# Performance work log

Hardware: AMD Instinct MI355X
Metric: run time of the kernel (lower is better)

Reference implementation:

```python
import jax, jax.numpy as jnp
import numpy as np

IGNORE_INDEX = -100
B, S, D, V = 4, 2048, 2048, 32000


def setup_inputs() -> dict:
    key = jax.random.key(0)
    k1, k2, k3, k4 = jax.random.split(key, 4)
    hidden = jax.random.normal(k1, (B, S, D), dtype=jnp.float32)
    targets = jax.random.randint(k2, (B, S), 0, V, dtype=jnp.int64)
    drop = jax.random.uniform(k3, (B, S)) < 0.1
    targets = jnp.where(drop, IGNORE_INDEX, targets)
    W = jax.random.normal(k4, (V, D), dtype=jnp.float32) * (D ** -0.5)
    return {"hidden": hidden, "targets": targets, "W": W}


def reference(hidden, targets, W):
    # hidden: [B, S, D], targets: [B, S] int, W: [V, D]
    mask = targets != IGNORE_INDEX                      # [B, S]
    total = mask.sum()
    # Linear projection to vocab, CE computed in fp32 (matches logits.float())
    logits = jnp.einsum('bsd,vd->bsv', hidden, W).astype(jnp.float32)  # [B, S, V]
    logp = jax.nn.log_softmax(logits, axis=-1)
    safe_t = jnp.where(mask, targets, 0)
    nll = -jnp.take_along_axis(logp, safe_t[..., None], axis=-1)[..., 0]  # [B, S]
    loss_sum = jnp.sum(jnp.where(mask, nll, 0.0))
    return loss_sum / total.astype(jnp.float32)
```

## Files before the change

### kernel.cpp

```cpp
#include <hip/hip_runtime.h>
#include <hip/hip_bf16.h>
#include <stdint.h>

#define IGNORE_INDEX (-100)

constexpr int M_ = 8192;
constexpr int K_ = 2048;
constexpr int N_ = 32000;

constexpr int BM = 128, BN = 128;

typedef __attribute__((ext_vector_type(4)))  float f32x4;
typedef __attribute__((ext_vector_type(16))) float f32x16;
typedef __attribute__((ext_vector_type(4)))  int   i32x4;
typedef __attribute__((ext_vector_type(8)))  int   i32x8;
typedef __attribute__((ext_vector_type(4)))  unsigned int u32x4;
typedef __attribute__((ext_vector_type(8)))  __bf16 bf16x8;

#define SCALE_A 8.0f
#define SCALE_W 1024.0f
#define INV_S   (1.0f / (8.0f * 1024.0f))

__device__ __forceinline__ unsigned pack_bf16(float f0, float f1) {
    unsigned u0 = __builtin_bit_cast(unsigned, f0) + 0x8000u;
    unsigned u1 = __builtin_bit_cast(unsigned, f1) + 0x8000u;
    return __builtin_amdgcn_perm(u1, u0, 0x07060302u);
}
__device__ __forceinline__ u32x4 pack8(f32x4 lo, f32x4 hi) {
    u32x4 r;
    r[0] = pack_bf16(lo[0], lo[1]);
    r[1] = pack_bf16(lo[2], lo[3]);
    r[2] = pack_bf16(hi[0], hi[1]);
    r[3] = pack_bf16(hi[2], hi[3]);
    return r;
}

__device__ __forceinline__ void gll16(const void* g, void* l) {
    __builtin_amdgcn_global_load_lds(
        (const __attribute__((address_space(1))) unsigned int*)g,
        (__attribute__((address_space(3))) unsigned int*)l, 16, 0, 0);
}

__global__ void init_acc(float* p, int n) {
    int i = blockIdx.x * 256 + threadIdx.x;
    if (i < n) p[i] = 0.0f;
}

__global__ __launch_bounds__(256) void convert_fp8(
    const float* __restrict__ in, unsigned int* __restrict__ out,
    float scale, int n8)
{
    int i = blockIdx.x * 256 + threadIdx.x;
    if (i < n8) {
        f32x4 lo = ((const f32x4*)in)[2 * i];
        f32x4 hi = ((const f32x4*)in)[2 * i + 1];
        int w0 = 0, w1 = 0;
        w0 = __builtin_amdgcn_cvt_pk_fp8_f32(lo[0] * scale, lo[1] * scale, w0, false);
        w0 = __builtin_amdgcn_cvt_pk_fp8_f32(lo[2] * scale, lo[3] * scale, w0, true);
        w1 = __builtin_amdgcn_cvt_pk_fp8_f32(hi[0] * scale, hi[1] * scale, w1, false);
        w1 = __builtin_amdgcn_cvt_pk_fp8_f32(hi[2] * scale, hi[3] * scale, w1, true);
        out[2 * i]     = (unsigned int)w0;
        out[2 * i + 1] = (unsigned int)w1;
    }
}

__global__ __launch_bounds__(512, 3) void gemm_fp8(
    const unsigned char* __restrict__ A,
    const unsigned char* __restrict__ Wq,
    const int*   __restrict__ tgt,
    float* __restrict__ sumexp,
    float* __restrict__ tgtlogit)
{
    __shared__ __align__(16) unsigned char As[BM * 64];
    __shared__ __align__(16) unsigned char Bs[BN * 64];
    __shared__ int tg[BM];

    const int tid = threadIdx.x;
    const int mt  = blockIdx.x;
    const int nt  = blockIdx.y;

    if (tid < BM) tg[tid] = tgt[mt * BM + tid];

    const int wave = tid >> 6;
    const int lane = tid & 63;
    const int wmo  = (wave & 3) * 32;
    const int wno  = (wave >> 2) * 64;

    const int srow = tid >> 2;
    const int spg  = (tid & 3) ^ ((srow >> 1) & 3);
    const unsigned char* gA = A  + (size_t)(mt * BM + srow) * K_ + spg * 16;
    const unsigned char* gB = Wq + (size_t)(nt * BN + srow) * K_ + spg * 16;
    unsigned char* lA = &As[wave * 1024];
    unsigned char* lB = &Bs[wave * 1024];

    const int l31 = lane & 31;
    const int h   = lane >> 5;
    const int ra  = wmo + l31;
    const int rb0 = wno + l31;
    const int rb1 = wno + 32 + l31;
    const int xa  = (ra  >> 1) & 3;
    const int xb0 = (rb0 >> 1) & 3;
    const int xb1 = (rb1 >> 1) & 3;
    const unsigned char* fA0 = &As[ra  * 64 + ((2 * h)     ^ xa ) * 16];
    const unsigned char* fA1 = &As[ra  * 64 + ((2 * h + 1) ^ xa ) * 16];
    const unsigned char* fB00 = &Bs[rb0 * 64 + ((2 * h)     ^ xb0) * 16];
    const unsigned char* fB01 = &Bs[rb0 * 64 + ((2 * h + 1) ^ xb0) * 16];
    const unsigned char* fB10 = &Bs[rb1 * 64 + ((2 * h)     ^ xb1) * 16];
    const unsigned char* fB11 = &Bs[rb1 * 64 + ((2 * h + 1) ^ xb1) * 16];

    f32x16 acc0, acc1;
#pragma unroll
    for (int r = 0; r < 16; r++) { acc0[r] = 0.f; acc1[r] = 0.f; }

#pragma unroll 1
    for (int kt = 0; kt < K_; kt += 64) {
        gll16(gA + kt, lA);
        gll16(gB + kt, lB);
        __syncthreads();

        i32x4 a_lo = *(const i32x4*)fA0;
        i32x4 a_hi = *(const i32x4*)fA1;
        i32x4 b0lo = *(const i32x4*)fB00;
        i32x4 b0hi = *(const i32x4*)fB01;
        i32x4 b1lo = *(const i32x4*)fB10;
        i32x4 b1hi = *(const i32x4*)fB11;
        i32x8 af = (i32x8){a_lo[0], a_lo[1], a_lo[2], a_lo[3],
                           a_hi[0], a_hi[1], a_hi[2], a_hi[3]};
        i32x8 bf0 = (i32x8){b0lo[0], b0lo[1], b0lo[2], b0lo[3],
                            b0hi[0], b0hi[1], b0hi[2], b0hi[3]};
        i32x8 bf1 = (i32x8){b1lo[0], b1lo[1], b1lo[2], b1lo[3],
                            b1hi[0], b1hi[1], b1hi[2], b1hi[3]};

        acc0 = __builtin_amdgcn_mfma_scale_f32_32x32x64_f8f6f4(
            af, bf0, acc0, 0, 0, 0, 0x7F7F7F7F, 0, 0x7F7F7F7F);
        acc1 = __builtin_amdgcn_mfma_scale_f32_32x32x64_f8f6f4(
            af, bf1, acc1, 0, 0, 0, 0x7F7F7F7F, 0, 0x7F7F7F7F);

        __syncthreads();
    }

    const int c0 = nt * BN + wno + l31;
#pragma unroll
    for (int reg = 0; reg < 16; reg++) {
        const int lrow = wmo + (reg & 3) + 8 * (reg >> 2) + 4 * h;
        const int grow = mt * BM + lrow;
        const int t    = tg[lrow];
        float v0 = acc0[reg] * INV_S;
        float v1 = acc1[reg] * INV_S;
        if (t == c0)      tgtlogit[grow] = v0;
        if (t == c0 + 32) tgtlogit[grow] = v1;
        float rs = __expf(v0) + __expf(v1);
        rs += __shfl_xor(rs, 1);
        rs += __shfl_xor(rs, 2);
        rs += __shfl_xor(rs, 4);
        rs += __shfl_xor(rs, 8);
        rs += __shfl_xor(rs, 16);
        if (l31 == 0) atomicAdd(&sumexp[grow], rs);
    }
}

constexpr int BKf = 32;
constexpr int LDA = BKf + 8;
__global__ __launch_bounds__(256) void gemm_fused_f32(
    const float* __restrict__ A,
    const float* __restrict__ W,
    const int*   __restrict__ tgt,
    float* __restrict__ sumexp,
    float* __restrict__ tgtlogit)
{
    __shared__ __bf16 As[BM * LDA];
    __shared__ __bf16 Bs[BN * LDA];
    __shared__ int    tg[BM];

    const int tid = threadIdx.x;
    const int mt  = blockIdx.x;
    const int nt  = blockIdx.y;
    if (tid < BM) tg[tid] = tgt[mt * BM + tid];

    const int wave = tid >> 6, lane = tid & 63;
    const int wm = wave >> 1, wn = wave & 1;
    const int lquad = lane >> 4, lcol = lane & 15;
    const int srow = tid >> 2, scol = (tid & 3) * 8;

    const float* gA = A + (size_t)(mt * BM + srow) * K_ + scol;
    const float* gB = W + (size_t)(nt * BN + srow) * K_ + scol;
    const size_t rowstep = (size_t)64 * K_;

    f32x4 acc[4][4];
#pragma unroll
    for (int i = 0; i < 4; i++)
#pragma unroll
        for (int j = 0; j < 4; j++) acc[i][j] = (f32x4){0.f, 0.f, 0.f, 0.f};

    for (int kt = 0; kt < K_; kt += BKf) {
        f32x4 a0 = *(const f32x4*)(gA + kt);
        f32x4 a1 = *(const f32x4*)(gA + kt + 4);
        f32x4 a2 = *(const f32x4*)(gA + kt + rowstep);
        f32x4 a3 = *(const f32x4*)(gA + kt + rowstep + 4);
        f32x4 b0 = *(const f32x4*)(gB + kt);
        f32x4 b1 = *(const f32x4*)(gB + kt + 4);
        f32x4 b2 = *(const f32x4*)(gB + kt + rowstep);
        f32x4 b3 = *(const f32x4*)(gB + kt + rowstep + 4);
        __syncthreads();
        *(u32x4*)&As[srow * LDA + scol]        = pack8(a0, a1);
        *(u32x4*)&As[(srow + 64) * LDA + scol] = pack8(a2, a3);
        *(u32x4*)&Bs[srow * LDA + scol]        = pack8(b0, b1);
        *(u32x4*)&Bs[(srow + 64) * LDA + scol] = pack8(b2, b3);
        __syncthreads();
        bf16x8 af[4], bf[4];
#pragma unroll
        for (int f = 0; f < 4; f++) {
            af[f] = *(const bf16x8*)&As[(wm * 64 + f * 16 + lcol) * LDA + lquad * 8];
            bf[f] = *(const bf16x8*)&Bs[(wn * 64 + f * 16 + lcol) * LDA + lquad * 8];
        }
#pragma unroll
        for (int mf = 0; mf < 4; mf++)
#pragma unroll
            for (int nf = 0; nf < 4; nf++)
                acc[mf][nf] = __builtin_amdgcn_mfma_f32_16x16x32_bf16(af[mf], bf[nf], acc[mf][nf], 0, 0, 0);
    }
    const int colbase = nt * BN + wn * 64;
#pragma unroll
    for (int mf = 0; mf < 4; mf++) {
#pragma unroll
        for (int r = 0; r < 4; r++) {
            const int lrow = wm * 64 + mf * 16 + lquad * 4 + r;
            const int grow = mt * BM + lrow;
            const int t    = tg[lrow];
            float rs = 0.f;
#pragma unroll
            for (int nf = 0; nf < 4; nf++) {
                float v = acc[mf][nf][r];
                rs += __expf(v);
                if (t == colbase + nf * 16 + lcol) tgtlogit[grow] = v;
            }
            rs += __shfl_xor(rs, 1);
            rs += __shfl_xor(rs, 2);
            rs += __shfl_xor(rs, 4);
            rs += __shfl_xor(rs, 8);
            if (lcol == 0) atomicAdd(&sumexp[grow], rs);
        }
    }
}

__global__ __launch_bounds__(256) void finalize(
    const float* __restrict__ sumexp,
    const float* __restrict__ tgtlogit,
    const int*   __restrict__ tgt,
    float* __restrict__ out)
{
    float s = 0.f;
    int   c = 0;
    for (int i = threadIdx.x; i < M_; i += 256) {
        int t = tgt[i];
        if (t != IGNORE_INDEX) {
            s += __logf(sumexp[i]) - tgtlogit[i];
            c++;
        }
    }
#pragma unroll
    for (int o = 32; o; o >>= 1) {
        s += __shfl_down(s, o);
        c += __shfl_down(c, o);
    }
    __shared__ float ss[4];
    __shared__ int   cc[4];
    int w = threadIdx.x >> 6;
    if ((threadIdx.x & 63) == 0) { ss[w] = s; cc[w] = c; }
    __syncthreads();
    if (threadIdx.x == 0) {
        float st = ss[0] + ss[1] + ss[2] + ss[3];
        int   ct = cc[0] + cc[1] + cc[2] + cc[3];
        out[0] = st / (float)ct;
    }
}

extern "C" void kernel_launch(void* const* d_in, const int* in_sizes, int n_in,
                              void* d_out, int out_size, void* d_ws, size_t ws_size,
                              hipStream_t stream) {
    const float* hidden  = (const float*)d_in[0];
    const int*   targets = (const int*)d_in[1];
    const float* W       = (const float*)d_in[2];

    float* sumexp   = (float*)d_ws;
    float* tgtlogit = sumexp + M_;
    float* out      = (float*)d_out;

    unsigned char* Aq = (unsigned char*)d_ws + 2 * M_ * sizeof(float);
    unsigned char* Wq = Aq + (size_t)M_ * K_;
    const size_t need = 2 * M_ * sizeof(float) + (size_t)M_ * K_ + (size_t)N_ * K_;

    init_acc<<<(2 * M_ + 255) / 256, 256, 0, stream>>>(sumexp, 2 * M_);

    if (ws_size >= need) {
        const int a8 = M_ * K_ / 8;
        const int w8 = N_ * K_ / 8;
        convert_fp8<<<(a8 + 255) / 256, 256, 0, stream>>>(hidden, (unsigned int*)Aq, SCALE_A, a8);
        convert_fp8<<<(w8 + 255) / 256, 256, 0, stream>>>(W, (unsigned int*)Wq, SCALE_W, w8);
        gemm_fp8<<<dim3(M_ / BM, N_ / BN), 512, 0, stream>>>(Aq, Wq, targets, sumexp, tgtlogit);
    } else {
        gemm_fused_f32<<<dim3(M_ / BM, N_ / BN), 256, 0, stream>>>(hidden, W, targets, sumexp, tgtlogit);
    }

    finalize<<<1, 256, 0, stream>>>(sumexp, tgtlogit, targets, out);
}
```

Baseline: 1.101 ms.

## Double-buffer fp8 GEMM LDS tiles and use 2x2 MFMA tiles per wave

Restructures the fp8 GEMM to use 256 threads with each wave computing a 64x64 sub-tile through four MFMAs, which raises register-level reuse of A and B fragments. LDS is double-buffered so the global-to-LDS loads for the next K slice are issued before computing the current one, aiming to hide memory latency behind MFMA work. It also raises wave priority around the MFMA block. The trade is more accumulator registers and twice the LDS per block, which may reduce occupancy.

```diff
diff --git a/kernel.cpp b/kernel.cpp
--- a/kernel.cpp
+++ b/kernel.cpp
@@ -64,15 +64,56 @@
     }
 }
 
-__global__ __launch_bounds__(512, 3) void gemm_fp8(
+
+#define MFMA_SC(a, b, c) \
+    __builtin_amdgcn_mfma_scale_f32_32x32x64_f8f6f4( \
+        (a), (b), (c), 0, 0, 0, 0x7F7F7F7F, 0, 0x7F7F7F7F)
+
+#define STAGE(asb, bsb, koff)                          \
+    do {                                               \
+        gll16(gA0 + (koff), (asb) + stoff);            \
+        gll16(gA1 + (koff), (asb) + stoff + 4096);     \
+        gll16(gB0 + (koff), (bsb) + stoff);            \
+        gll16(gB1 + (koff), (bsb) + stoff + 4096);     \
+    } while (0)
+
+#define COMPUTE(asb, bsb)                                                     \
+    do {                                                                      \
+        const unsigned char* pA_ = (asb);                                     \
+        const unsigned char* pB_ = (bsb);                                     \
+        i32x4 aL0 = *(const i32x4*)(pA_ + aoffL);                             \
+        i32x4 aH0 = *(const i32x4*)(pA_ + aoffH);                             \
+        i32x4 aL1 = *(const i32x4*)(pA_ + aoffL + 2048);                      \
+        i32x4 aH1 = *(const i32x4*)(pA_ + aoffH + 2048);                      \
+        i32x4 bL0 = *(const i32x4*)(pB_ + boffL);                             \
+        i32x4 bH0 = *(const i32x4*)(pB_ + boffH);                             \
+        i32x4 bL1 = *(const i32x4*)(pB_ + boffL + 2048);                      \
+        i32x4 bH1 = *(const i32x4*)(pB_ + boffH + 2048);                      \
+        i32x8 af0 = (i32x8){aL0[0], aL0[1], aL0[2], aL0[3],                   \
+                            aH0[0], aH0[1], aH0[2], aH0[3]};                  \
+        i32x8 af1 = (i32x8){aL1[0], aL1[1], aL1[2], aL1[3],                   \
+                            aH1[0], aH1[1], aH1[2], aH1[3]};                  \
+        i32x8 bf0 = (i32x8){bL0[0], bL0[1], bL0[2], bL0[3],                   \
+                            bH0[0], bH0[1], bH0[2], bH0[3]};                  \
+        i32x8 bf1 = (i32x8){bL1[0], bL1[1], bL1[2], bL1[3],                   \
+                            bH1[0], bH1[1], bH1[2], bH1[3]};                  \
+        __builtin_amdgcn_s_setprio(1);                                        \
+        acc00 = MFMA_SC(af0, bf0, acc00);                                     \
+        acc01 = MFMA_SC(af0, bf1, acc01);                                     \
+        acc10 = MFMA_SC(af1, bf0, acc10);                                     \
+        acc11 = MFMA_SC(af1, bf1, acc11);                                     \
+        __builtin_amdgcn_s_setprio(0);                                        \
+    } while (0)
+
+__global__ __launch_bounds__(256, 3) void gemm_fp8(
     const unsigned char* __restrict__ A,
     const unsigned char* __restrict__ Wq,
     const int*   __restrict__ tgt,
     float* __restrict__ sumexp,
     float* __restrict__ tgtlogit)
 {
-    __shared__ __align__(16) unsigned char As[BM * 64];
-    __shared__ __align__(16) unsigned char Bs[BN * 64];
+    __shared__ __align__(16) unsigned char As[2][BM * 64];
+    __shared__ __align__(16) unsigned char Bs[2][BN * 64];
     __shared__ int tg[BM];
 
     const int tid = threadIdx.x;
@@ -83,79 +124,86 @@
 
     const int wave = tid >> 6;
     const int lane = tid & 63;
-    const int wmo  = (wave & 3) * 32;
-    const int wno  = (wave >> 2) * 64;
+    const int wm   = wave >> 1;
+    const int wn   = wave & 1;
 
     const int srow = tid >> 2;
     const int spg  = (tid & 3) ^ ((srow >> 1) & 3);
-    const unsigned char* gA = A  + (size_t)(mt * BM + srow) * K_ + spg * 16;
-    const unsigned char* gB = Wq + (size_t)(nt * BN + srow) * K_ + spg * 16;
-    unsigned char* lA = &As[wave * 1024];
-    unsigned char* lB = &Bs[wave * 1024];
+    const unsigned char* gA0 = A  + (size_t)(mt * BM + srow) * K_ + spg * 16;
+    const unsigned char* gB0 = Wq + (size_t)(nt * BN + srow) * K_ + spg * 16;
+    const unsigned char* gA1 = gA0 + (size_t)64 * K_;
+    const unsigned char* gB1 = gB0 + (size_t)64 * K_;
+    const int stoff = wave * 1024;
 
     const int l31 = lane & 31;
     const int h   = lane >> 5;
-    const int ra  = wmo + l31;
-    const int rb0 = wno + l31;
-    const int rb1 = wno + 32 + l31;
-    const int xa  = (ra  >> 1) & 3;
-    const int xb0 = (rb0 >> 1) & 3;
-    const int xb1 = (rb1 >> 1) & 3;
-    const unsigned char* fA0 = &As[ra  * 64 + ((2 * h)     ^ xa ) * 16];
-    const unsigned char* fA1 = &As[ra  * 64 + ((2 * h + 1) ^ xa ) * 16];
-    const unsigned char* fB00 = &Bs[rb0 * 64 + ((2 * h)     ^ xb0) * 16];
-    const unsigned char* fB01 = &Bs[rb0 * 64 + ((2 * h + 1) ^ xb0) * 16];
-    const unsigned char* fB10 = &Bs[rb1 * 64 + ((2 * h)     ^ xb1) * 16];
-    const unsigned char* fB11 = &Bs[rb1 * 64 + ((2 * h + 1) ^ xb1) * 16];
-
-    f32x16 acc0, acc1;
-#pragma unroll
-    for (int r = 0; r < 16; r++) { acc0[r] = 0.f; acc1[r] = 0.f; }
+    const int ra  = wm * 64 + l31;
+    const int rb  = wn * 64 + l31;
+    const int xa  = (ra >> 1) & 3;
+    const int xb  = (rb >> 1) & 3;
+    const int aoffL = ra * 64 + ((2 * h)     ^ xa) * 16;
+    const int aoffH = ra * 64 + ((2 * h + 1) ^ xa) * 16;
+    const int boffL = rb * 64 + ((2 * h)     ^ xb) * 16;
+    const int boffH = rb * 64 + ((2 * h + 1) ^ xb) * 16;
+
+    f32x16 acc00, acc01, acc10, acc11;
+#pragma unroll
+    for (int r = 0; r < 16; r++) {
+        acc00[r] = 0.f; acc01[r] = 0.f; acc10[r] = 0.f; acc11[r] = 0.f;
+    }
+
+    STAGE(As[0], Bs[0], 0);
+    __syncthreads();
 
 #pragma unroll 1
-    for (int kt = 0; kt < K_; kt += 64) {
-        gll16(gA + kt, lA);
-        gll16(gB + kt, lB);
+    for (int kt = 0; kt < K_; kt += 128) {
+        STAGE(As[1], Bs[1], kt + 64);
+        __builtin_amdgcn_sched_barrier(0);
+        COMPUTE(As[0], Bs[0]);
         __syncthreads();
 
-        i32x4 a_lo = *(const i32x4*)fA0;
-        i32x4 a_hi = *(const i32x4*)fA1;
-        i32x4 b0lo = *(const i32x4*)fB00;
-        i32x4 b0hi = *(const i32x4*)fB01;
-        i32x4 b1lo = *(const i32x4*)fB10;
-        i32x4 b1hi = *(const i32x4*)fB11;
-        i32x8 af = (i32x8){a_lo[0], a_lo[1], a_lo[2], a_lo[3],
-                           a_hi[0], a_hi[1], a_hi[2], a_hi[3]};
-        i32x8 bf0 = (i32x8){b0lo[0], b0lo[1], b0lo[2], b0lo[3],
-                            b0hi[0], b0hi[1], b0hi[2], b0hi[3]};
-        i32x8 bf1 = (i32x8){b1lo[0], b1lo[1], b1lo[2], b1lo[3],
-                            b1hi[0], b1hi[1], b1hi[2], b1hi[3]};
-
-        acc0 = __builtin_amdgcn_mfma_scale_f32_32x32x64_f8f6f4(
-            af, bf0, acc0, 0, 0, 0, 0x7F7F7F7F, 0, 0x7F7F7F7F);
-        acc1 = __builtin_amdgcn_mfma_scale_f32_32x32x64_f8f6f4(
-            af, bf1, acc1, 0, 0, 0, 0x7F7F7F7F, 0, 0x7F7F7F7F);
-
+        if (kt + 128 < K_) STAGE(As[0], Bs[0], kt + 128);
+        __builtin_amdgcn_sched_barrier(0);
+        COMPUTE(As[1], Bs[1]);
         __syncthreads();
     }
 
-    const int c0 = nt * BN + wno + l31;
+    const int c0 = nt * BN + wn * 64 + l31;
 #pragma unroll
     for (int reg = 0; reg < 16; reg++) {
-        const int lrow = wmo + (reg & 3) + 8 * (reg >> 2) + 4 * h;
-        const int grow = mt * BM + lrow;
-        const int t    = tg[lrow];
-        float v0 = acc0[reg] * INV_S;
-        float v1 = acc1[reg] * INV_S;
-        if (t == c0)      tgtlogit[grow] = v0;
-        if (t == c0 + 32) tgtlogit[grow] = v1;
-        float rs = __expf(v0) + __expf(v1);
-        rs += __shfl_xor(rs, 1);
-        rs += __shfl_xor(rs, 2);
-        rs += __shfl_xor(rs, 4);
-        rs += __shfl_xor(rs, 8);
-        rs += __shfl_xor(rs, 16);
-        if (l31 == 0) atomicAdd(&sumexp[grow], rs);
+        const int rbase = (reg & 3) + 8 * (reg >> 2) + 4 * h;
+        {
+            const int lrow = wm * 64 + rbase;
+            const int grow = mt * BM + lrow;
+            const int t    = tg[lrow];
+            float v0 = acc00[reg] * INV_S;
+            float v1 = acc01[reg] * INV_S;
+            if (t == c0)      tgtlogit[grow] = v0;
+            if (t == c0 + 32) tgtlogit[grow] = v1;
+            float rs = __expf(v0) + __expf(v1);
+            rs += __shfl_xor(rs, 1);
+            rs += __shfl_xor(rs, 2);
+            rs += __shfl_xor(rs, 4);
+            rs += __shfl_xor(rs, 8);
+            rs += __shfl_xor(rs, 16);
+            if (l31 == 0) atomicAdd(&sumexp[grow], rs);
+        }
+        {
+            const int lrow = wm * 64 + 32 + rbase;
+            const int grow = mt * BM + lrow;
+            const int t    = tg[lrow];
+            float v0 = acc10[reg] * INV_S;
+            float v1 = acc11[reg] * INV_S;
+            if (t == c0)      tgtlogit[grow] = v0;
+            if (t == c0 + 32) tgtlogit[grow] = v1;
+            float rs = __expf(v0) + __expf(v1);
+            rs += __shfl_xor(rs, 1);
+            rs += __shfl_xor(rs, 2);
+            rs += __shfl_xor(rs, 4);
+            rs += __shfl_xor(rs, 8);
+            rs += __shfl_xor(rs, 16);
+            if (l31 == 0) atomicAdd(&sumexp[grow], rs);
+        }
     }
 }
 
@@ -297,7 +345,7 @@
         const int w8 = N_ * K_ / 8;
         convert_fp8<<<(a8 + 255) / 256, 256, 0, stream>>>(hidden, (unsigned int*)Aq, SCALE_A, a8);
         convert_fp8<<<(w8 + 255) / 256, 256, 0, stream>>>(W, (unsigned int*)Wq, SCALE_W, w8);
-        gemm_fp8<<<dim3(M_ / BM, N_ / BN), 512, 0, stream>>>(Aq, Wq, targets, sumexp, tgtlogit);
+        gemm_fp8<<<dim3(M_ / BM, N_ / BN), 256, 0, stream>>>(Aq, Wq, targets, sumexp, tgtlogit);
     } else {
         gemm_fused_f32<<<dim3(M_ / BM, N_ / BN), 256, 0, stream>>>(hidden, W, targets, sumexp, tgtlogit);
     }
```

New measurement: 1.082 ms. No clear change (-1.7%).

## Enlarge FP8 GEMM tile to 256x256 with double-buffered pipelined LDS loads

Applied to the files above, without the earlier changes.

Reworks the FP8 MFMA GEMM to use 256x256 block tiles, with each wave computing a 128x64 sub-tile (4x2 MFMAs). LDS is double-buffered so global-to-LDS loads for the next k-tile are issued between MFMA groups, using fine-grained barriers, waitcnts and setprio. The 1D grid is remapped so consecutive blocks are spread across XCDs. This targets the old kernel's low arithmetic intensity and its full sync stalls on every k-step. In exchange it uses more registers and LDS (occupancy drops to 2 blocks), and the hand-written barrier and waitcnt ordering is fragile.

```diff
diff --git a/kernel.cpp b/kernel.cpp
--- a/kernel.cpp
+++ b/kernel.cpp
@@ -7,8 +7,6 @@
 constexpr int M_ = 8192;
 constexpr int K_ = 2048;
 constexpr int N_ = 32000;
-
-constexpr int BM = 128, BN = 128;
 
 typedef __attribute__((ext_vector_type(4)))  float f32x4;
 typedef __attribute__((ext_vector_type(16))) float f32x16;
@@ -64,101 +62,187 @@
     }
 }
 
-__global__ __launch_bounds__(512, 3) void gemm_fp8(
+
+#define MFMA_SC(a, b, c) \
+    __builtin_amdgcn_mfma_scale_f32_32x32x64_f8f6f4( \
+        (a), (b), (c), 0, 0, 0, 0x7F7F7F7F, 0, 0x7F7F7F7F)
+
+#define CAT8(lo, hi) (i32x8){(lo)[0], (lo)[1], (lo)[2], (lo)[3], \
+                             (hi)[0], (hi)[1], (hi)[2], (hi)[3]}
+
+#define LGKM0() do { \
+    asm volatile("s_waitcnt lgkmcnt(0)" ::: "memory"); \
+    __builtin_amdgcn_sched_barrier(0); \
+} while (0)
+
+template <bool STA, bool STB, int BVM>
+__device__ __forceinline__ void ktile(
+    const unsigned char* cA, const unsigned char* cB,
+    unsigned char* nA, unsigned char* sB,
+    const unsigned char* gAlo, const unsigned char* gAhi, int koffA,
+    const unsigned char* gBlo, const unsigned char* gBhi, int koffB,
+    int stoff, int aoffL, int aoffH, int boffL, int boffH,
+    f32x16 (&acc)[4][2])
+{
+    i32x4 aL0 = *(const i32x4*)(cA + aoffL);
+    i32x4 aH0 = *(const i32x4*)(cA + aoffH);
+    i32x4 aL1 = *(const i32x4*)(cA + aoffL + 2048);
+    i32x4 aH1 = *(const i32x4*)(cA + aoffH + 2048);
+    i32x4 bL0 = *(const i32x4*)(cB + boffL);
+    i32x4 bH0 = *(const i32x4*)(cB + boffH);
+    if (STA) gll16(gAlo + koffA, nA + stoff);
+    __builtin_amdgcn_s_barrier();
+    LGKM0();
+    i32x8 af0 = CAT8(aL0, aH0);
+    i32x8 af1 = CAT8(aL1, aH1);
+    i32x8 bf0 = CAT8(bL0, bH0);
+    __builtin_amdgcn_s_setprio(1);
+    acc[0][0] = MFMA_SC(af0, bf0, acc[0][0]);
+    acc[1][0] = MFMA_SC(af1, bf0, acc[1][0]);
+    __builtin_amdgcn_s_setprio(0);
+    __builtin_amdgcn_s_barrier();
+
+    i32x4 bL1 = *(const i32x4*)(cB + boffL + 2048);
+    i32x4 bH1 = *(const i32x4*)(cB + boffH + 2048);
+    if (STA) gll16(gAhi + koffA, nA + 8192 + stoff);
+    __builtin_amdgcn_s_barrier();
+    LGKM0();
+    i32x8 bf1 = CAT8(bL1, bH1);
+    __builtin_amdgcn_s_setprio(1);
+    acc[0][1] = MFMA_SC(af0, bf1, acc[0][1]);
+    acc[1][1] = MFMA_SC(af1, bf1, acc[1][1]);
+    __builtin_amdgcn_s_setprio(0);
+    __builtin_amdgcn_s_barrier();
+
+    i32x4 aL2 = *(const i32x4*)(cA + aoffL + 4096);
+    i32x4 aH2 = *(const i32x4*)(cA + aoffH + 4096);
+    i32x4 aL3 = *(const i32x4*)(cA + aoffL + 6144);
+    i32x4 aH3 = *(const i32x4*)(cA + aoffH + 6144);
+    if (STB) gll16(gBlo + koffB, sB + stoff);
+    __builtin_amdgcn_s_barrier();
+    LGKM0();
+    i32x8 af2 = CAT8(aL2, aH2);
+    i32x8 af3 = CAT8(aL3, aH3);
+    __builtin_amdgcn_s_setprio(1);
+    acc[2][0] = MFMA_SC(af2, bf0, acc[2][0]);
+    acc[3][0] = MFMA_SC(af3, bf0, acc[3][0]);
+    __builtin_amdgcn_s_setprio(0);
+    __builtin_amdgcn_s_barrier();
+
+    if (STB) gll16(gBhi + koffB, sB + 8192 + stoff);
+    __builtin_amdgcn_s_barrier();
+    __builtin_amdgcn_s_setprio(1);
+    acc[2][1] = MFMA_SC(af2, bf1, acc[2][1]);
+    acc[3][1] = MFMA_SC(af3, bf1, acc[3][1]);
+    __builtin_amdgcn_s_setprio(0);
+    if constexpr (BVM == 0) {
+        asm volatile("s_waitcnt vmcnt(0)" ::: "memory");
+    } else if constexpr (BVM == 2) {
+        asm volatile("s_waitcnt vmcnt(2)" ::: "memory");
+    }
+    __builtin_amdgcn_s_barrier();
+}
+
+__global__ __launch_bounds__(512, 2) void gemm_fp8(
     const unsigned char* __restrict__ A,
     const unsigned char* __restrict__ Wq,
     const int*   __restrict__ tgt,
     float* __restrict__ sumexp,
     float* __restrict__ tgtlogit)
 {
-    __shared__ __align__(16) unsigned char As[BM * 64];
-    __shared__ __align__(16) unsigned char Bs[BN * 64];
-    __shared__ int tg[BM];
+    __shared__ __align__(16) unsigned char As[2][16384];
+    __shared__ __align__(16) unsigned char Bs[2][16384];
+    __shared__ int tg[256];
 
     const int tid = threadIdx.x;
-    const int mt  = blockIdx.x;
-    const int nt  = blockIdx.y;
-
-    if (tid < BM) tg[tid] = tgt[mt * BM + tid];
+
+    const int b  = blockIdx.x;
+    const int b2 = (b & 7) * 500 + (b >> 3);
+    const int mt = b2 & 31;
+    const int nt = b2 >> 5;
+
+    if (tid < 256) tg[tid] = tgt[mt * 256 + tid];
 
     const int wave = tid >> 6;
     const int lane = tid & 63;
-    const int wmo  = (wave & 3) * 32;
-    const int wno  = (wave >> 2) * 64;
+    const int wm   = wave >> 2;
+    const int wn   = wave & 3;
 
     const int srow = tid >> 2;
     const int spg  = (tid & 3) ^ ((srow >> 1) & 3);
-    const unsigned char* gA = A  + (size_t)(mt * BM + srow) * K_ + spg * 16;
-    const unsigned char* gB = Wq + (size_t)(nt * BN + srow) * K_ + spg * 16;
-    unsigned char* lA = &As[wave * 1024];
-    unsigned char* lB = &Bs[wave * 1024];
+    const unsigned char* gAlo = A  + (size_t)(mt * 256 + srow) * K_ + spg * 16;
+    const unsigned char* gAhi = gAlo + (size_t)128 * K_;
+    const unsigned char* gBlo = Wq + (size_t)(nt * 256 + srow) * K_ + spg * 16;
+    const unsigned char* gBhi = gBlo + (size_t)128 * K_;
+    const int stoff = wave * 1024;
 
     const int l31 = lane & 31;
     const int h   = lane >> 5;
-    const int ra  = wmo + l31;
-    const int rb0 = wno + l31;
-    const int rb1 = wno + 32 + l31;
-    const int xa  = (ra  >> 1) & 3;
-    const int xb0 = (rb0 >> 1) & 3;
-    const int xb1 = (rb1 >> 1) & 3;
-    const unsigned char* fA0 = &As[ra  * 64 + ((2 * h)     ^ xa ) * 16];
-    const unsigned char* fA1 = &As[ra  * 64 + ((2 * h + 1) ^ xa ) * 16];
-    const unsigned char* fB00 = &Bs[rb0 * 64 + ((2 * h)     ^ xb0) * 16];
-    const unsigned char* fB01 = &Bs[rb0 * 64 + ((2 * h + 1) ^ xb0) * 16];
-    const unsigned char* fB10 = &Bs[rb1 * 64 + ((2 * h)     ^ xb1) * 16];
-    const unsigned char* fB11 = &Bs[rb1 * 64 + ((2 * h + 1) ^ xb1) * 16];
-
-    f32x16 acc0, acc1;
-#pragma unroll
-    for (int r = 0; r < 16; r++) { acc0[r] = 0.f; acc1[r] = 0.f; }
+    const int x   = (l31 >> 1) & 3;
+    const int aoffL = (wm * 128 + l31) * 64 + ((2 * h)     ^ x) * 16;
+    const int aoffH = (wm * 128 + l31) * 64 + ((2 * h + 1) ^ x) * 16;
+    const int boffL = (wn * 64  + l31) * 64 + ((2 * h)     ^ x) * 16;
+    const int boffH = (wn * 64  + l31) * 64 + ((2 * h + 1) ^ x) * 16;
+
+    f32x16 acc[4][2];
+#pragma unroll
+    for (int m = 0; m < 4; m++)
+#pragma unroll
+        for (int n = 0; n < 2; n++)
+#pragma unroll
+            for (int r = 0; r < 16; r++) acc[m][n][r] = 0.f;
+
+    gll16(gAlo,      As[0] + stoff);
+    gll16(gAhi,      As[0] + 8192 + stoff);
+    gll16(gBlo,      Bs[0] + stoff);
+    gll16(gBhi,      Bs[0] + 8192 + stoff);
+    gll16(gBlo + 64, Bs[1] + stoff);
+    gll16(gBhi + 64, Bs[1] + 8192 + stoff);
+    asm volatile("s_waitcnt vmcnt(2) lgkmcnt(0)" ::: "memory");
+    __builtin_amdgcn_s_barrier();
 
 #pragma unroll 1
-    for (int kt = 0; kt < K_; kt += 64) {
-        gll16(gA + kt, lA);
-        gll16(gB + kt, lB);
-        __syncthreads();
-
-        i32x4 a_lo = *(const i32x4*)fA0;
-        i32x4 a_hi = *(const i32x4*)fA1;
-        i32x4 b0lo = *(const i32x4*)fB00;
-        i32x4 b0hi = *(const i32x4*)fB01;
-        i32x4 b1lo = *(const i32x4*)fB10;
-        i32x4 b1hi = *(const i32x4*)fB11;
-        i32x8 af = (i32x8){a_lo[0], a_lo[1], a_lo[2], a_lo[3],
-                           a_hi[0], a_hi[1], a_hi[2], a_hi[3]};
-        i32x8 bf0 = (i32x8){b0lo[0], b0lo[1], b0lo[2], b0lo[3],
-                            b0hi[0], b0hi[1], b0hi[2], b0hi[3]};
-        i32x8 bf1 = (i32x8){b1lo[0], b1lo[1], b1lo[2], b1lo[3],
-                            b1hi[0], b1hi[1], b1hi[2], b1hi[3]};
-
-        acc0 = __builtin_amdgcn_mfma_scale_f32_32x32x64_f8f6f4(
-            af, bf0, acc0, 0, 0, 0, 0x7F7F7F7F, 0, 0x7F7F7F7F);
-        acc1 = __builtin_amdgcn_mfma_scale_f32_32x32x64_f8f6f4(
-            af, bf1, acc1, 0, 0, 0, 0x7F7F7F7F, 0, 0x7F7F7F7F);
-
-        __syncthreads();
-    }
-
-    const int c0 = nt * BN + wno + l31;
-#pragma unroll
-    for (int reg = 0; reg < 16; reg++) {
-        const int lrow = wmo + (reg & 3) + 8 * (reg >> 2) + 4 * h;
-        const int grow = mt * BM + lrow;
-        const int t    = tg[lrow];
-        float v0 = acc0[reg] * INV_S;
-        float v1 = acc1[reg] * INV_S;
-        if (t == c0)      tgtlogit[grow] = v0;
-        if (t == c0 + 32) tgtlogit[grow] = v1;
-        float rs = __expf(v0) + __expf(v1);
-        rs += __shfl_xor(rs, 1);
-        rs += __shfl_xor(rs, 2);
-        rs += __shfl_xor(rs, 4);
-        rs += __shfl_xor(rs, 8);
-        rs += __shfl_xor(rs, 16);
-        if (l31 == 0) atomicAdd(&sumexp[grow], rs);
-    }
-}
-
+    for (int it = 0; it < 15; ++it) {
+        ktile<true, true, 2>(As[0], Bs[0], As[1], Bs[0],
+                             gAlo, gAhi, 64, gBlo, gBhi, 128,
+                             stoff, aoffL, aoffH, boffL, boffH, acc);
+        ktile<true, true, 2>(As[1], Bs[1], As[0], Bs[1],
+                             gAlo, gAhi, 128, gBlo, gBhi, 192,
+                             stoff, aoffL, aoffH, boffL, boffH, acc);
+        gAlo += 128; gAhi += 128; gBlo += 128; gBhi += 128;
+    }
+    ktile<true, false, 0>(As[0], Bs[0], As[1], Bs[0],
+                          gAlo, gAhi, 64, gBlo, gBhi, 0,
+                          stoff, aoffL, aoffH, boffL, boffH, acc);
+    ktile<false, false, -1>(As[1], Bs[1], As[0], Bs[1],
+                            gAlo, gAhi, 0, gBlo, gBhi, 0,
+                            stoff, aoffL, aoffH, boffL, boffH, acc);
+
+    const int c0 = nt * 256 + wn * 64 + l31;
+#pragma unroll
+    for (int ms = 0; ms < 4; ++ms) {
+#pragma unroll
+        for (int reg = 0; reg < 16; ++reg) {
+            const int rbase = (reg & 3) + 8 * (reg >> 2) + 4 * h;
+            const int lrow  = wm * 128 + ms * 32 + rbase;
+            const int grow  = mt * 256 + lrow;
+            const int t     = tg[lrow];
+            float v0 = acc[ms][0][reg] * INV_S;
+            float v1 = acc[ms][1][reg] * INV_S;
+            if (t == c0)      tgtlogit[grow] = v0;
+            if (t == c0 + 32) tgtlogit[grow] = v1;
+            float rs = __expf(v0) + __expf(v1);
+            rs += __shfl_xor(rs, 1);
+            rs += __shfl_xor(rs, 2);
+            rs += __shfl_xor(rs, 4);
+            rs += __shfl_xor(rs, 8);
+            rs += __shfl_xor(rs, 16);
+            if (l31 == 0) atomicAdd(&sumexp[grow], rs);
+        }
+    }
+}
+
+constexpr int BMf = 128, BNf = 128;
 constexpr int BKf = 32;
 constexpr int LDA = BKf + 8;
 __global__ __launch_bounds__(256) void gemm_fused_f32(
@@ -168,22 +252,22 @@
     float* __restrict__ sumexp,
     float* __restrict__ tgtlogit)
 {
-    __shared__ __bf16 As[BM * LDA];
-    __shared__ __bf16 Bs[BN * LDA];
-    __shared__ int    tg[BM];
+    __shared__ __bf16 As[BMf * LDA];
+    __shared__ __bf16 Bs[BNf * LDA];
+    __shared__ int    tg[BMf];
 
     const int tid = threadIdx.x;
     const int mt  = blockIdx.x;
     const int nt  = blockIdx.y;
-    if (tid < BM) tg[tid] = tgt[mt * BM + tid];
+    if (tid < BMf) tg[tid] = tgt[mt * BMf + tid];
 
     const int wave = tid >> 6, lane = tid & 63;
     const int wm = wave >> 1, wn = wave & 1;
     const int lquad = lane >> 4, lcol = lane & 15;
     const int srow = tid >> 2, scol = (tid & 3) * 8;
 
-    const float* gA = A + (size_t)(mt * BM + srow) * K_ + scol;
-    const float* gB = W + (size_t)(nt * BN + srow) * K_ + scol;
+    const float* gA = A + (size_t)(mt * BMf + srow) * K_ + scol;
+    const float* gB = W + (size_t)(nt * BNf + srow) * K_ + scol;
     const size_t rowstep = (size_t)64 * K_;
 
     f32x4 acc[4][4];
@@ -219,13 +303,13 @@
             for (int nf = 0; nf < 4; nf++)
                 acc[mf][nf] = __builtin_amdgcn_mfma_f32_16x16x32_bf16(af[mf], bf[nf], acc[mf][nf], 0, 0, 0);
     }
-    const int colbase = nt * BN + wn * 64;
+    const int colbase = nt * BNf + wn * 64;
 #pragma unroll
     for (int mf = 0; mf < 4; mf++) {
 #pragma unroll
         for (int r = 0; r < 4; r++) {
             const int lrow = wm * 64 + mf * 16 + lquad * 4 + r;
-            const int grow = mt * BM + lrow;
+            const int grow = mt * BMf + lrow;
             const int t    = tg[lrow];
             float rs = 0.f;
 #pragma unroll
@@ -297,9 +381,9 @@
         const int w8 = N_ * K_ / 8;
         convert_fp8<<<(a8 + 255) / 256, 256, 0, stream>>>(hidden, (unsigned int*)Aq, SCALE_A, a8);
         convert_fp8<<<(w8 + 255) / 256, 256, 0, stream>>>(W, (unsigned int*)Wq, SCALE_W, w8);
-        gemm_fp8<<<dim3(M_ / BM, N_ / BN), 512, 0, stream>>>(Aq, Wq, targets, sumexp, tgtlogit);
+        gemm_fp8<<<(M_ / 256) * (N_ / 256), 512, 0, stream>>>(Aq, Wq, targets, sumexp, tgtlogit);
     } else {
-        gemm_fused_f32<<<dim3(M_ / BM, N_ / BN), 256, 0, stream>>>(hidden, W, targets, sumexp, tgtlogit);
+        gemm_fused_f32<<<dim3(M_ / BMf, N_ / BNf), 256, 0, stream>>>(hidden, W, targets, sumexp, tgtlogit);
     }
 
     finalize<<<1, 256, 0, stream>>>(sumexp, tgtlogit, targets, out);
```

After: 1.299 ms. 1.18x slower.
